# Kernel tuning notes

Hardware: AMD Instinct MI355X
Metric: run time of the kernel (lower is better)

Reference implementation:

```python
import jax, jax.numpy as jnp
import numpy as np

N_NODES = 50000
N_EDGES = 800000
D = 64  # node/edge feature dim == out_dim


def _dense_params(key, d_in, d_out):
    kw, kb = jax.random.split(key)
    # flax Dense default: lecun_normal kernel, zero bias
    W = jax.random.normal(kw, (d_in, d_out), dtype=jnp.float32) / np.sqrt(d_in)
    b = jnp.zeros((d_out,), dtype=jnp.float32)
    return W, b


def setup_inputs() -> dict:
    key = jax.random.key(0)
    ks = jax.random.split(key, 10)
    nodes = jax.random.normal(ks[0], (N_NODES, D), dtype=jnp.float32)
    edges = jax.random.normal(ks[1], (N_EDGES, D), dtype=jnp.float32)
    senders = jax.random.randint(ks[2], (N_EDGES,), 0, N_NODES, dtype=jnp.int32)
    receivers = jax.random.randint(ks[3], (N_EDGES,), 0, N_NODES, dtype=jnp.int32)
    W_sent, b_sent = _dense_params(ks[4], D, D)      # sent_attributes_1
    W_recv, b_recv = _dense_params(ks[5], D, D)      # received_attributes
    W_edge, b_edge = _dense_params(ks[6], D, D)      # edge projection
    W_attn, b_attn = _dense_params(ks[7], D, 1)      # attention logit
    W_msg,  b_msg  = _dense_params(ks[8], D, D)      # message Dense (simple_update)
    W_self, b_self = _dense_params(ks[9], D, D)      # self-edge Dense
    return {
        "nodes": nodes, "edges": edges, "senders": senders, "receivers": receivers,
        "W_sent": W_sent, "b_sent": b_sent, "W_recv": W_recv, "b_recv": b_recv,
        "W_edge": W_edge, "b_edge": b_edge, "W_attn": W_attn, "b_attn": b_attn,
        "W_msg": W_msg, "b_msg": b_msg, "W_self": W_self, "b_self": b_self,
    }


def _segment_softmax(logits, segment_ids, num_segments):
    # logits: [E, 1]; stable softmax within each receiver segment
    maxs = jax.ops.segment_max(logits, segment_ids, num_segments=num_segments)
    ex = jnp.exp(logits - maxs[segment_ids])
    sums = jax.ops.segment_sum(ex, segment_ids, num_segments=num_segments)
    return ex / sums[segment_ids]


def reference(nodes, edges, senders, receivers,
              W_sent, b_sent, W_recv, b_recv, W_edge, b_edge,
              W_attn, b_attn, W_msg, b_msg, W_self, b_self):
    # Defaults: simple_update=True -> sync_updates=False, add_features=True,
    # mix_edge_node=False, self_edges=True.
    sent1 = (nodes @ W_sent + b_sent)[senders]          # [E, D]
    sent2 = nodes[senders]                              # [E, D] (simple_update)
    recv  = (nodes @ W_recv + b_recv)[receivers]        # [E, D]
    edge_feat = edges @ W_edge + b_edge                 # [E, D]
    edge_feat = sent1 + edge_feat + recv                # add_features
    logits = jax.nn.leaky_relu(edge_feat @ W_attn + b_attn)   # [E, 1]
    attn = _segment_softmax(logits, receivers, nodes.shape[0])  # [E, 1]
    message = sent2 @ W_msg + b_msg                     # [E, D]
    message = attn * message
    new_nodes = jax.ops.segment_sum(message, receivers, num_segments=nodes.shape[0])
    new_nodes = new_nodes + (nodes @ W_self + b_self)   # self_edges
    return new_nodes, edge_feat
```

## Files before the change

kernel.cpp:

```cpp
#include <hip/hip_runtime.h>
#include <math.h>

constexpr int NN = 50000;
constexpr int NE = 800000;
constexpr int DD = 64;

__device__ __forceinline__ float wave_max(float v) {
    #pragma unroll
    for (int off = 32; off > 0; off >>= 1) v = fmaxf(v, __shfl_xor(v, off, 64));
    return v;
}
__device__ __forceinline__ float wave_sum(float v) {
    #pragma unroll
    for (int off = 32; off > 0; off >>= 1) v += __shfl_xor(v, off, 64);
    return v;
}

__device__ __forceinline__ void gemm_row(const float* __restrict__ xrow,
                                         const float* __restrict__ W,
                                         float acc[DD]) {
    for (int kc = 0; kc < 4; ++kc) {
        float4 x0 = *(const float4*)(xrow + kc * 16 + 0);
        float4 x1 = *(const float4*)(xrow + kc * 16 + 4);
        float4 x2 = *(const float4*)(xrow + kc * 16 + 8);
        float4 x3 = *(const float4*)(xrow + kc * 16 + 12);
        float xs[16] = {x0.x, x0.y, x0.z, x0.w, x1.x, x1.y, x1.z, x1.w,
                        x2.x, x2.y, x2.z, x2.w, x3.x, x3.y, x3.z, x3.w};
        #pragma unroll
        for (int kk = 0; kk < 16; ++kk) {
            const float* Wr = W + (kc * 16 + kk) * DD;
            #pragma unroll
            for (int j = 0; j < DD; ++j) acc[j] = fmaf(xs[kk], Wr[j], acc[j]);
        }
    }
}

__global__ void k_init(int* __restrict__ deg) {
    int i = blockIdx.x * blockDim.x + threadIdx.x;
    if (i < NN) deg[i] = 0;
}

__global__ void k_count(const int* __restrict__ receivers, int* __restrict__ deg) {
    int e = blockIdx.x * blockDim.x + threadIdx.x;
    if (e < NE) atomicAdd(deg + receivers[e], 1);
}

__global__ __launch_bounds__(1024) void k_scan(const int* __restrict__ deg,
                                               int* __restrict__ starts) {
    __shared__ int buf0[1024], buf1[1024];
    const int t = threadIdx.x;
    constexpr int C = (NN + 1023) / 1024;
    int lo = t * C; if (lo > NN) lo = NN;
    int hi = lo + C; if (hi > NN) hi = NN;
    int s = 0;
    for (int i = lo; i < hi; ++i) s += deg[i];
    buf0[t] = s;
    __syncthreads();
    int* src = buf0; int* dst = buf1;
    for (int off = 1; off < 1024; off <<= 1) {
        int v = src[t] + ((t >= off) ? src[t - off] : 0);
        dst[t] = v;
        __syncthreads();
        int* tmp = src; src = dst; dst = tmp;
    }
    int run = (t == 0) ? 0 : src[t - 1];
    for (int i = lo; i < hi; ++i) { starts[i] = run; run += deg[i]; }
}

__global__ void k_fill(const int* __restrict__ receivers,
                       int* __restrict__ starts, int* __restrict__ eidx) {
    int e = blockIdx.x * blockDim.x + threadIdx.x;
    if (e < NE) {
        int pos = atomicAdd(starts + receivers[e], 1);
        eidx[pos] = e;
    }
}

__global__ __launch_bounds__(256, 2) void k_node(
    const float* __restrict__ nodes,
    const float* __restrict__ Wsent, const float* __restrict__ bsent,
    const float* __restrict__ Wrecv, const float* __restrict__ brecv,
    const float* __restrict__ Wmsg,  const float* __restrict__ bmsg,
    const float* __restrict__ Wself, const float* __restrict__ bself,
    float* __restrict__ sentP, float* __restrict__ recvP,
    float* __restrict__ msgP,  float* __restrict__ selfOut) {
    const int lane = threadIdx.x & 63;
    const int w    = (blockIdx.x * 256 + threadIdx.x) >> 6;
    const int m    = w & 3;
    const int tile = w >> 2;
    const int iRaw = tile * 64 + lane;
    const int i    = iRaw < NN ? iRaw : NN - 1;

    const float* W; const float* bias; float* out;
    if (m == 0)      { W = Wsent; bias = bsent; out = sentP; }
    else if (m == 1) { W = Wrecv; bias = brecv; out = recvP; }
    else if (m == 2) { W = Wmsg;  bias = bmsg;  out = msgP; }
    else             { W = Wself; bias = bself; out = selfOut; }

    float acc[DD];
    #pragma unroll
    for (int j = 0; j < DD; ++j) acc[j] = bias[j];

    gemm_row(nodes + (size_t)i * DD, W, acc);

    if (iRaw < NN) {
        float* orow = out + (size_t)i * DD;
        #pragma unroll
        for (int j4 = 0; j4 < DD / 4; ++j4) {
            float4 v; v.x = acc[j4*4+0]; v.y = acc[j4*4+1];
                      v.z = acc[j4*4+2]; v.w = acc[j4*4+3];
            *(float4*)(orow + j4 * 4) = v;
        }
    }
}

__global__ __launch_bounds__(256, 2) void k_edge(
    const float* __restrict__ edges,
    const int* __restrict__ senders, const int* __restrict__ receivers,
    const float* __restrict__ Wedge, const float* __restrict__ bedge,
    const float* __restrict__ Wattn, const float* __restrict__ battn,
    const float* __restrict__ sentP, const float* __restrict__ recvP,
    float* __restrict__ edgeOut, float* __restrict__ logits) {
    const int lane = threadIdx.x & 63;
    const int w = (blockIdx.x * 256 + threadIdx.x) >> 6;
    const int e = w * 64 + lane;

    float acc[DD];
    #pragma unroll
    for (int j = 0; j < DD; ++j) acc[j] = bedge[j];

    gemm_row(edges + (size_t)e * DD, Wedge, acc);

    const int s = senders[e];
    const int r = receivers[e];
    const float* srow = sentP + (size_t)s * DD;
    const float* rrow = recvP + (size_t)r * DD;
    float* orow = edgeOut + (size_t)e * DD;
    float t = 0.0f;
    #pragma unroll
    for (int j4 = 0; j4 < DD / 4; ++j4) {
        float4 sv = *(const float4*)(srow + j4 * 4);
        float4 rv = *(const float4*)(rrow + j4 * 4);
        float4 ev;
        ev.x = acc[j4*4+0] + sv.x + rv.x;
        ev.y = acc[j4*4+1] + sv.y + rv.y;
        ev.z = acc[j4*4+2] + sv.z + rv.z;
        ev.w = acc[j4*4+3] + sv.w + rv.w;
        t += ev.x * Wattn[j4*4+0] + ev.y * Wattn[j4*4+1]
           + ev.z * Wattn[j4*4+2] + ev.w * Wattn[j4*4+3];
        *(float4*)(orow + j4 * 4) = ev;
    }
    float v = t + battn[0];
    v = v > 0.0f ? v : 0.01f * v;
    logits[e] = v;
}

__global__ void k_final(
    const int* __restrict__ ends, const int* __restrict__ eidx,
    const int* __restrict__ senders, const float* __restrict__ logits,
    const float* __restrict__ msgP, float* __restrict__ outNodes) {
    const int lane = threadIdx.x & 63;
    const int n = (blockIdx.x * 256 + threadIdx.x) >> 6;
    if (n >= NN) return;
    const int end = ends[n];
    const int beg = (n > 0) ? ends[n - 1] : 0;
    if (end == beg) return;

    float mloc = -1e30f;
    for (int b = beg + lane; b < end; b += 64)
        mloc = fmaxf(mloc, logits[eidx[b]]);
    const float m = wave_max(mloc);

    float sloc = 0.0f;
    for (int b = beg + lane; b < end; b += 64)
        sloc += expf(logits[eidx[b]] - m);
    const float inv = 1.0f / wave_sum(sloc);

    float acc0 = 0.0f, acc1 = 0.0f;
    int b = beg;
    for (; b + 2 <= end; b += 2) {
        const int e0 = eidx[b], e1 = eidx[b + 1];
        const int s0 = senders[e0], s1 = senders[e1];
        const float w0 = expf(logits[e0] - m);
        const float w1 = expf(logits[e1] - m);
        acc0 += w0 * msgP[(size_t)s0 * DD + lane];
        acc1 += w1 * msgP[(size_t)s1 * DD + lane];
    }
    if (b < end) {
        const int e0 = eidx[b];
        acc0 += expf(logits[e0] - m) * msgP[(size_t)senders[e0] * DD + lane];
    }
    outNodes[(size_t)n * DD + lane] += (acc0 + acc1) * inv;
}

extern "C" void kernel_launch(void* const* d_in, const int* in_sizes, int n_in,
                              void* d_out, int out_size, void* d_ws, size_t ws_size,
                              hipStream_t stream) {
    const float* nodes     = (const float*)d_in[0];
    const float* edges     = (const float*)d_in[1];
    const int*   senders   = (const int*)d_in[2];
    const int*   receivers = (const int*)d_in[3];
    const float* Wsent = (const float*)d_in[4];
    const float* bsent = (const float*)d_in[5];
    const float* Wrecv = (const float*)d_in[6];
    const float* brecv = (const float*)d_in[7];
    const float* Wedge = (const float*)d_in[8];
    const float* bedge = (const float*)d_in[9];
    const float* Wattn = (const float*)d_in[10];
    const float* battn = (const float*)d_in[11];
    const float* Wmsg  = (const float*)d_in[12];
    const float* bmsg  = (const float*)d_in[13];
    const float* Wself = (const float*)d_in[14];
    const float* bself = (const float*)d_in[15];

    float* out = (float*)d_out;
    float* outNodes = out;
    float* outEdge  = out + (size_t)NN * DD;

    float* ws = (float*)d_ws;
    float* sentP  = ws;
    float* recvP  = sentP + (size_t)NN * DD;
    float* msgP   = recvP + (size_t)NN * DD;
    float* logits = msgP  + (size_t)NN * DD;
    int*   deg    = (int*)(logits + NE);
    int*   starts = deg + NN;
    int*   eidx   = starts + NN;

    k_init <<<(NN + 255) / 256, 256, 0, stream>>>(deg);
    k_count<<<(NE + 255) / 256, 256, 0, stream>>>(receivers, deg);
    k_scan <<<1, 1024, 0, stream>>>(deg, starts);
    k_fill <<<(NE + 255) / 256, 256, 0, stream>>>(receivers, starts, eidx);
    k_node <<<782, 256, 0, stream>>>(nodes, Wsent, bsent, Wrecv, brecv,
                                     Wmsg, bmsg, Wself, bself,
                                     sentP, recvP, msgP, outNodes);
    k_edge <<<3125, 256, 0, stream>>>(edges, senders, receivers, Wedge, bedge,
                                      Wattn, battn, sentP, recvP,
                                      outEdge, logits);
    k_final<<<(NN * 64 + 255) / 256, 256, 0, stream>>>(starts, eidx, senders,
                                                       logits, msgP, outNodes);
}
```

Baseline: 986.4 us.

## Remap node/edge GEMMs to lane-per-output-column with register-resident weights and grid-stride rows

Reworks k_node and k_edge so each wave processes one row at a time with each lane owning one output column. Each lane keeps its 64-entry weight column in registers across a grid-stride loop, replacing the old thread-per-row layout that held 64 accumulators and issued strided per-thread row loads. Row loads become wave-uniform broadcasts and output stores become fully coalesced. The attention logit is now a wave shuffle reduction. The trade-off is per-row wave serialisation, an extra reduction per edge, and new grid sizes.

```diff
diff --git a/kernel.cpp b/kernel.cpp
--- a/kernel.cpp
+++ b/kernel.cpp
@@ -16,24 +16,27 @@
     return v;
 }
 
-__device__ __forceinline__ void gemm_row(const float* __restrict__ xrow,
-                                         const float* __restrict__ W,
-                                         float acc[DD]) {
-    for (int kc = 0; kc < 4; ++kc) {
-        float4 x0 = *(const float4*)(xrow + kc * 16 + 0);
-        float4 x1 = *(const float4*)(xrow + kc * 16 + 4);
-        float4 x2 = *(const float4*)(xrow + kc * 16 + 8);
-        float4 x3 = *(const float4*)(xrow + kc * 16 + 12);
-        float xs[16] = {x0.x, x0.y, x0.z, x0.w, x1.x, x1.y, x1.z, x1.w,
-                        x2.x, x2.y, x2.z, x2.w, x3.x, x3.y, x3.z, x3.w};
-        #pragma unroll
-        for (int kk = 0; kk < 16; ++kk) {
-            const float* Wr = W + (kc * 16 + kk) * DD;
-            #pragma unroll
-            for (int j = 0; j < DD; ++j) acc[j] = fmaf(xs[kk], Wr[j], acc[j]);
-        }
-    }
-}
+
+#define LOADW(c) const float4 wc##c = make_float4( \
+    W[(4*(c)+0)*DD + lane], W[(4*(c)+1)*DD + lane], \
+    W[(4*(c)+2)*DD + lane], W[(4*(c)+3)*DD + lane]);
+
+#define LOADW_ALL \
+    LOADW(0) LOADW(1) LOADW(2)  LOADW(3)  LOADW(4)  LOADW(5)  LOADW(6)  LOADW(7) \
+    LOADW(8) LOADW(9) LOADW(10) LOADW(11) LOADW(12) LOADW(13) LOADW(14) LOADW(15)
+
+#define STEP(c, acc) { \
+    const float4 xv = *(const float4*)(xrow + 4*(c)); \
+    acc = fmaf(xv.x, wc##c.x, acc); \
+    acc = fmaf(xv.y, wc##c.y, acc); \
+    acc = fmaf(xv.z, wc##c.z, acc); \
+    acc = fmaf(xv.w, wc##c.w, acc); }
+
+#define STEP_ALL \
+    STEP(0,a0)  STEP(1,a1)  STEP(2,a2)  STEP(3,a3) \
+    STEP(4,a0)  STEP(5,a1)  STEP(6,a2)  STEP(7,a3) \
+    STEP(8,a0)  STEP(9,a1)  STEP(10,a2) STEP(11,a3) \
+    STEP(12,a0) STEP(13,a1) STEP(14,a2) STEP(15,a3)
 
 __global__ void k_init(int* __restrict__ deg) {
     int i = blockIdx.x * blockDim.x + threadIdx.x;
@@ -85,11 +88,11 @@
     float* __restrict__ sentP, float* __restrict__ recvP,
     float* __restrict__ msgP,  float* __restrict__ selfOut) {
     const int lane = threadIdx.x & 63;
-    const int w    = (blockIdx.x * 256 + threadIdx.x) >> 6;
-    const int m    = w & 3;
-    const int tile = w >> 2;
-    const int iRaw = tile * 64 + lane;
-    const int i    = iRaw < NN ? iRaw : NN - 1;
+    const int wid  = (blockIdx.x * 256 + threadIdx.x) >> 6;
+    const int nw   = (gridDim.x * 256) >> 6;
+    const int m    = wid & 3;
+    const int wsub = wid >> 2;
+    const int nsub = nw >> 2;
 
     const float* W; const float* bias; float* out;
     if (m == 0)      { W = Wsent; bias = bsent; out = sentP; }
@@ -97,20 +100,15 @@
     else if (m == 2) { W = Wmsg;  bias = bmsg;  out = msgP; }
     else             { W = Wself; bias = bself; out = selfOut; }
 
-    float acc[DD];
-    #pragma unroll
-    for (int j = 0; j < DD; ++j) acc[j] = bias[j];
-
-    gemm_row(nodes + (size_t)i * DD, W, acc);
-
-    if (iRaw < NN) {
-        float* orow = out + (size_t)i * DD;
-        #pragma unroll
-        for (int j4 = 0; j4 < DD / 4; ++j4) {
-            float4 v; v.x = acc[j4*4+0]; v.y = acc[j4*4+1];
-                      v.z = acc[j4*4+2]; v.w = acc[j4*4+3];
-            *(float4*)(orow + j4 * 4) = v;
-        }
+    LOADW_ALL
+    const float b = bias[lane];
+
+    for (int i0 = wsub; i0 < NN; i0 += nsub) {
+        const int i = __builtin_amdgcn_readfirstlane(i0);
+        const float* xrow = nodes + (size_t)i * DD;
+        float a0 = b, a1 = 0.0f, a2 = 0.0f, a3 = 0.0f;
+        STEP_ALL
+        out[(size_t)i * DD + lane] = (a0 + a1) + (a2 + a3);
     }
 }
 
@@ -122,37 +120,35 @@
     const float* __restrict__ sentP, const float* __restrict__ recvP,
     float* __restrict__ edgeOut, float* __restrict__ logits) {
     const int lane = threadIdx.x & 63;
-    const int w = (blockIdx.x * 256 + threadIdx.x) >> 6;
-    const int e = w * 64 + lane;
-
-    float acc[DD];
-    #pragma unroll
-    for (int j = 0; j < DD; ++j) acc[j] = bedge[j];
-
-    gemm_row(edges + (size_t)e * DD, Wedge, acc);
-
-    const int s = senders[e];
-    const int r = receivers[e];
-    const float* srow = sentP + (size_t)s * DD;
-    const float* rrow = recvP + (size_t)r * DD;
-    float* orow = edgeOut + (size_t)e * DD;
-    float t = 0.0f;
-    #pragma unroll
-    for (int j4 = 0; j4 < DD / 4; ++j4) {
-        float4 sv = *(const float4*)(srow + j4 * 4);
-        float4 rv = *(const float4*)(rrow + j4 * 4);
-        float4 ev;
-        ev.x = acc[j4*4+0] + sv.x + rv.x;
-        ev.y = acc[j4*4+1] + sv.y + rv.y;
-        ev.z = acc[j4*4+2] + sv.z + rv.z;
-        ev.w = acc[j4*4+3] + sv.w + rv.w;
-        t += ev.x * Wattn[j4*4+0] + ev.y * Wattn[j4*4+1]
-           + ev.z * Wattn[j4*4+2] + ev.w * Wattn[j4*4+3];
-        *(float4*)(orow + j4 * 4) = ev;
-    }
-    float v = t + battn[0];
-    v = v > 0.0f ? v : 0.01f * v;
-    logits[e] = v;
+    const int wid  = (blockIdx.x * 256 + threadIdx.x) >> 6;
+    const int nw   = (gridDim.x * 256) >> 6;
+    const float* W = Wedge;
+
+    LOADW_ALL
+    const float be = bedge[lane];
+    const float wa = Wattn[lane];
+    const float ba = battn[0];
+
+    for (int e0 = wid; e0 < NE; e0 += nw) {
+        const int e = __builtin_amdgcn_readfirstlane(e0);
+        const int s = senders[e];
+        const int r = receivers[e];
+        const float g0 = sentP[(size_t)s * DD + lane];
+        const float g1 = recvP[(size_t)r * DD + lane];
+        const float* xrow = edges + (size_t)e * DD;
+        float a0 = be, a1 = g0 + g1, a2 = 0.0f, a3 = 0.0f;
+        STEP_ALL
+        const float ef = (a0 + a1) + (a2 + a3);
+        edgeOut[(size_t)e * DD + lane] = ef;
+        float t = ef * wa;
+        #pragma unroll
+        for (int off = 32; off > 0; off >>= 1) t += __shfl_xor(t, off, 64);
+        if (lane == 0) {
+            float v = t + ba;
+            v = v > 0.0f ? v : 0.01f * v;
+            logits[e] = v;
+        }
+    }
 }
 
 __global__ void k_final(
@@ -230,10 +226,10 @@
     k_count<<<(NE + 255) / 256, 256, 0, stream>>>(receivers, deg);
     k_scan <<<1, 1024, 0, stream>>>(deg, starts);
     k_fill <<<(NE + 255) / 256, 256, 0, stream>>>(receivers, starts, eidx);
-    k_node <<<782, 256, 0, stream>>>(nodes, Wsent, bsent, Wrecv, brecv,
-                                     Wmsg, bmsg, Wself, bself,
-                                     sentP, recvP, msgP, outNodes);
-    k_edge <<<3125, 256, 0, stream>>>(edges, senders, receivers, Wedge, bedge,
+    k_node <<<1024, 256, 0, stream>>>(nodes, Wsent, bsent, Wrecv, brecv,
+                                      Wmsg, bmsg, Wself, bself,
+                                      sentP, recvP, msgP, outNodes);
+    k_edge <<<4096, 256, 0, stream>>>(edges, senders, receivers, Wedge, bedge,
                                       Wattn, battn, sentP, recvP,
                                       outEdge, logits);
     k_final<<<(NN * 64 + 255) / 256, 256, 0, stream>>>(starts, eidx, senders,
```

Result: slower. 1.012 ms (+2.6%).
